# Optimization experiments

Hardware: AMD Instinct MI355X
Metric: run time of the kernel (lower is better)

## Reference

```python
import jax, jax.numpy as jnp
import numpy as np

S = 1024   # speakers_per_batch
U = 64     # utterances_per_speaker
D = 256    # embedding_size
EPS = 1e-5


def setup_inputs() -> dict:
    key = jax.random.key(0)
    k1, = jax.random.split(key, 1)
    return {
        "output_of_model": jax.random.normal(k1, (S * U, D), dtype=jnp.float32),
        "similarity_weight": jnp.array([10.0], dtype=jnp.float32),
        "similarity_bias": jnp.array([-5.0], dtype=jnp.float32),
        "speakers_per_batch": S,
        "utterances_per_speaker": U,
    }


def reference(output_of_model, similarity_weight, similarity_bias,
              speakers_per_batch, utterances_per_speaker):
    s, u = speakers_per_batch, utterances_per_speaker
    embeds = output_of_model.reshape(s, u, -1)                      # [S,U,D]

    # inclusive centroids (mean over utterances, L2-normalized with +eps)
    c_incl = jnp.mean(embeds, axis=1)                               # [S,D]
    c_incl = c_incl / (jnp.linalg.norm(c_incl, axis=-1, keepdims=True) + EPS)

    # exclusive centroids (leave-one-out mean, L2-normalized with +eps)
    c_excl = (jnp.sum(embeds, axis=1, keepdims=True) - embeds) / (u - 1)  # [S,U,D]
    c_excl = c_excl / (jnp.linalg.norm(c_excl, axis=-1, keepdims=True) + EPS)

    # normalized embeddings (original normalizes embeds inside the loop)
    e_n = embeds / (jnp.linalg.norm(embeds, axis=-1, keepdims=True) + EPS)

    # off-diagonal: cosine(embed[i,u], incl centroid[j]); diagonal: excl centroid
    sim_incl = jnp.einsum('sud,jd->suj', e_n, c_incl)               # [S,U,S]
    sim_excl = jnp.sum(e_n * c_excl, axis=-1)                       # [S,U]
    diag = jnp.eye(s, dtype=bool)[:, None, :]                       # [S,1,S]
    sim = jnp.where(diag, sim_excl[:, :, None], sim_incl)           # [S,U,S]

    sim = sim * similarity_weight + similarity_bias                 # scaled logits

    logits = sim.reshape(s * u, s)
    targets = jnp.repeat(jnp.arange(s), u)                          # ground truth
    logp = jax.nn.log_softmax(logits, axis=-1)
    loss = -jnp.mean(jnp.take_along_axis(logp, targets[:, None], axis=-1))
    return loss
```

## Files before the change

### kernel.cpp

```cpp
#include <hip/hip_runtime.h>

#define SPK 1024
#define UTT 64
#define DIM 256
#define EPSV 1e-5f
#define NROW (SPK * UTT)
#define NSL 8
#define LOG2E 1.44269504f

typedef __attribute__((ext_vector_type(4))) float f32x4;
typedef __attribute__((ext_vector_type(2))) long long2v;

#define EXP2(x) __builtin_amdgcn_exp2f(x)

__device__ __forceinline__ int pk_fp8(float a, float b, float c, float d) {
    int v = __builtin_amdgcn_cvt_pk_fp8_f32(a, b, 0, false);
    return  __builtin_amdgcn_cvt_pk_fp8_f32(c, d, v, true);
}

__device__ __forceinline__ int fragIdx(int g) {
    return ((g >> 4) * 4 + ((g & 7) >> 1)) * 4 + ((g >> 3) & 1) * 2 + (g & 1);
}

__global__ __launch_bounds__(256)
void k_prep(const float* __restrict__ x,
            unsigned char* __restrict__ cincl8,
            unsigned char* __restrict__ en8,
            float* __restrict__ texcl,
            const float* __restrict__ wp, const float* __restrict__ bp) {
    __shared__ float4 sc4[256];
    __shared__ float4 cs4[64];
    __shared__ float sccs;
    int s = blockIdx.x, tid = threadIdx.x;
    int dq = tid & 63, ug = tid >> 6;
    const float4* x4 = (const float4*)(x + (size_t)s * UTT * DIM);

    float4 p = {0.f, 0.f, 0.f, 0.f};
#pragma unroll
    for (int i = 0; i < 16; ++i) {
        float4 v = x4[(ug * 16 + i) * 64 + dq];
        p.x += v.x; p.y += v.y; p.z += v.z; p.w += v.w;
    }
    sc4[tid] = p;
    __syncthreads();
    if (tid < 64) {
        float4 a = sc4[dq], b2 = sc4[64 + dq], c = sc4[128 + dq], d = sc4[192 + dq];
        float4 cs = {a.x + b2.x + c.x + d.x, a.y + b2.y + c.y + d.y,
                     a.z + b2.z + c.z + d.z, a.w + b2.w + c.w + d.w};
        cs4[dq] = cs;
        float s2 = cs.x * cs.x + cs.y * cs.y + cs.z * cs.z + cs.w * cs.w;
#pragma unroll
        for (int o = 1; o < 64; o <<= 1) s2 += __shfl_xor(s2, o);
        if (tid == 0) sccs = s2;
        float inv = 16.f / (sqrtf(s2) + UTT * EPSV);
        ((int*)cincl8)[s * 64 + fragIdx(dq)] =
            pk_fp8(cs.x * inv, cs.y * inv, cs.z * inv, cs.w * inv);
    }
    __syncthreads();
    float scc = sccs;
    float w = wp[0], b = bp[0];

    int row = tid >> 2, sub = tid & 3;
    const float4* xr = x4 + row * 64;
    float4 xv[16];
    float sx = 0.f, sc = 0.f;
#pragma unroll
    for (int i = 0; i < 16; ++i) {
        float4 v = xr[i * 4 + sub];
        float4 cv = cs4[i * 4 + sub];
        xv[i] = v;
        sx += v.x * v.x + v.y * v.y + v.z * v.z + v.w * v.w;
        sc += v.x * cv.x + v.y * cv.y + v.z * cv.z + v.w * cv.w;
    }
    sx += __shfl_xor(sx, 1); sx += __shfl_xor(sx, 2);
    sc += __shfl_xor(sc, 1); sc += __shfl_xor(sc, 2);
    float nx = sqrtf(sx);
    float inv = 16.f / (nx + EPSV);
    int* er = (int*)(en8 + (size_t)(s * UTT + row) * DIM);
#pragma unroll
    for (int i = 0; i < 16; ++i)
        er[fragIdx(i * 4 + sub)] = pk_fp8(xv[i].x * inv, xv[i].y * inv,
                                          xv[i].z * inv, xv[i].w * inv);
    if (sub == 0) {
        float num = sc - sx;
        float e2 = fmaxf(scc - 2.f * sc + sx, 0.f);
        float sim = num / ((nx + EPSV) * (sqrtf(e2) + (UTT - 1) * EPSV));
        texcl[s * UTT + row] = fmaf(sim, w, b);
    }
}

__global__ __launch_bounds__(256, 3)
void k_main(const unsigned char* __restrict__ en8,
            const unsigned char* __restrict__ cincl8,
            float* __restrict__ partial,
            const float* __restrict__ wp, const float* __restrict__ bp) {
    __shared__ unsigned char Bs[32 * 1024];
    int tid = threadIdx.x, wave = tid >> 6, lane = tid & 63;
    int quad = lane >> 4, lx = lane & 15;
    int bid = blockIdx.x;
    int xcd = bid & 7, j = bid >> 3;
    int cs = j & 7;
    int sg = xcd + 8 * (j >> 3);
    int sw = sg * 4 + wave;
    float w = wp[0], b = bp[0];
    float M  = fabsf(w) * 1.0625f + b;
    float wl = w * (LOG2E / 256.f);
    float bl = (b - M) * LOG2E;

#pragma unroll
    for (int nti = 0; nti < 2; ++nti) {
        int nt = wave * 2 + nti;
#pragma unroll
        for (int r = 0; r < 4; ++r) {
            const unsigned char* g = cincl8 +
                (size_t)(cs * 128 + nt * 16 + lx) * DIM + (r * 4 + quad) * 16;
            __builtin_amdgcn_global_load_lds(
                (const __attribute__((address_space(1))) void*)g,
                (__attribute__((address_space(3))) void*)(Bs + (nt * 4 + r) * 1024),
                16, 0, 0);
        }
    }

    const unsigned char* abase = en8 + (size_t)sw * UTT * DIM;
    long2v af2[4][4];
#pragma unroll
    for (int mt = 0; mt < 4; ++mt)
#pragma unroll
        for (int r = 0; r < 4; ++r)
            af2[mt][r] = *(const long2v*)(abase + (mt * 16 + lx) * DIM + (r * 4 + quad) * 16);

    float l[16];
#pragma unroll
    for (int i = 0; i < 16; ++i) l[i] = 0.f;

    __syncthreads();

    int dnt = (sw >> 4) - cs * 8;
    int dlx = sw & 15;

    for (int nt = 0; nt < 8; ++nt) {
        long2v bf2[4];
#pragma unroll
        for (int r = 0; r < 4; ++r)
            bf2[r] = *(const long2v*)(Bs + (nt * 4 + r) * 1024 + lane * 16);
        f32x4 aA[4] = {{0.f,0.f,0.f,0.f},{0.f,0.f,0.f,0.f},
                       {0.f,0.f,0.f,0.f},{0.f,0.f,0.f,0.f}};
        f32x4 aB[4] = {{0.f,0.f,0.f,0.f},{0.f,0.f,0.f,0.f},
                       {0.f,0.f,0.f,0.f},{0.f,0.f,0.f,0.f}};
#pragma unroll
        for (int r = 0; r < 2; ++r) {
#pragma unroll
            for (int mt = 0; mt < 4; ++mt) {
                aA[mt] = __builtin_amdgcn_mfma_f32_16x16x32_fp8_fp8(af2[mt][r].x,   bf2[r].x,   aA[mt], 0, 0, 0);
                aB[mt] = __builtin_amdgcn_mfma_f32_16x16x32_fp8_fp8(af2[mt][r+2].x, bf2[r+2].x, aB[mt], 0, 0, 0);
            }
#pragma unroll
            for (int mt = 0; mt < 4; ++mt) {
                aA[mt] = __builtin_amdgcn_mfma_f32_16x16x32_fp8_fp8(af2[mt][r].y,   bf2[r].y,   aA[mt], 0, 0, 0);
                aB[mt] = __builtin_amdgcn_mfma_f32_16x16x32_fp8_fp8(af2[mt][r+2].y, bf2[r+2].y, aB[mt], 0, 0, 0);
            }
        }
#pragma unroll
        for (int mt = 0; mt < 4; ++mt)
#pragma unroll
            for (int r = 0; r < 4; ++r)
                l[mt * 4 + r] += EXP2(fmaf(aA[mt][r] + aB[mt][r], wl, bl));
        if (nt == dnt) {
#pragma unroll
            for (int mt = 0; mt < 4; ++mt)
#pragma unroll
                for (int r = 0; r < 4; ++r) {
                    float e = EXP2(fmaf(aA[mt][r] + aB[mt][r], wl, bl));
                    if (lx == dlx) l[mt * 4 + r] -= e;
                }
        }
    }

#pragma unroll
    for (int o = 1; o < 16; o <<= 1)
#pragma unroll
        for (int i = 0; i < 16; ++i) l[i] += __shfl_xor(l[i], o);
    if (lx == 0)
#pragma unroll
        for (int mt = 0; mt < 4; ++mt)
#pragma unroll
            for (int r = 0; r < 4; ++r)
                partial[(size_t)cs * NROW + (size_t)sw * UTT + mt * 16 + quad * 4 + r]
                    = l[mt * 4 + r];
}

__global__ __launch_bounds__(256)
void k_final(const float* __restrict__ partial, const float* __restrict__ texcl,
             const float* __restrict__ wp, const float* __restrict__ bp,
             float* __restrict__ out) {
    int row = blockIdx.x * 256 + threadIdx.x;
    float w = wp[0], b = bp[0];
    float M = fabsf(w) * 1.0625f + b;
    float t = 0.f;
#pragma unroll
    for (int sl = 0; sl < NSL; ++sl) t += partial[(size_t)sl * NROW + row];
    float tex = texcl[row];
    float c = (M + __logf(t + EXP2((tex - M) * LOG2E))) - tex;
#pragma unroll
    for (int o = 1; o < 64; o <<= 1) c += __shfl_xor(c, o);
    __shared__ float red[4];
    if ((threadIdx.x & 63) == 0) red[threadIdx.x >> 6] = c;
    __syncthreads();
    if (threadIdx.x == 0)
        atomicAdd(out, (red[0] + red[1] + red[2] + red[3]) * (1.f / NROW));
}

extern "C" void kernel_launch(void* const* d_in, const int* in_sizes, int n_in,
                              void* d_out, int out_size, void* d_ws, size_t ws_size,
                              hipStream_t stream) {
    const float* x  = (const float*)d_in[0];
    const float* wp = (const float*)d_in[1];
    const float* bp = (const float*)d_in[2];
    char* ws = (char*)d_ws;
    unsigned char* cincl8 = (unsigned char*)ws;
    float* texcl          = (float*)(ws + (1u << 19));
    float* partial        = (float*)(ws + (1u << 20));
    unsigned char* en8    = (unsigned char*)(ws + (4u << 20));
    float* out = (float*)d_out;

    hipMemsetAsync(d_out, 0, sizeof(float), stream);
    k_prep <<<SPK, 256, 0, stream>>>(x, cincl8, en8, texcl, wp, bp);
    k_main <<<(SPK / 4) * NSL, 256, 0, stream>>>(en8, cincl8, partial, wp, bp);
    k_final<<<NROW / 256, 256, 0, stream>>>(partial, texcl, wp, bp, out);
}
```

Baseline: 142.7 us.

## Fuse embedding normalization, GEMM and logsumexp into one kernel per speaker

Restructures the pipeline from prep/main/final into a centroid kernel plus a fused kernel. The fused kernel loads raw fp32 rows, computes norms and the exclusive similarity, and quantizes to fp8 in registers. It then streams all 1024 centroids through double-buffered LDS and finishes the log-softmax and loss reduction in place. This removes the fp8 embedding buffer round trip, the partial-sum array and the final kernel launch. In exchange, each block now handles only 64 rows with a single accumulator per wave, which gives less MFMA reuse and adds a sync per tile, and the input x is read from memory twice.

```diff
diff --git a/kernel.cpp b/kernel.cpp
--- a/kernel.cpp
+++ b/kernel.cpp
@@ -5,7 +5,6 @@
 #define DIM 256
 #define EPSV 1e-5f
 #define NROW (SPK * UTT)
-#define NSL 8
 #define LOG2E 1.44269504f
 
 typedef __attribute__((ext_vector_type(4))) float f32x4;
@@ -23,18 +22,12 @@
 }
 
 __global__ __launch_bounds__(256)
-void k_prep(const float* __restrict__ x,
-            unsigned char* __restrict__ cincl8,
-            unsigned char* __restrict__ en8,
-            float* __restrict__ texcl,
-            const float* __restrict__ wp, const float* __restrict__ bp) {
+void k_cent(const float* __restrict__ x, unsigned char* __restrict__ cincl8,
+            float* __restrict__ csum, float* __restrict__ nrm) {
     __shared__ float4 sc4[256];
-    __shared__ float4 cs4[64];
-    __shared__ float sccs;
     int s = blockIdx.x, tid = threadIdx.x;
     int dq = tid & 63, ug = tid >> 6;
     const float4* x4 = (const float4*)(x + (size_t)s * UTT * DIM);
-
     float4 p = {0.f, 0.f, 0.f, 0.f};
 #pragma unroll
     for (int i = 0; i < 16; ++i) {
@@ -47,166 +40,130 @@
         float4 a = sc4[dq], b2 = sc4[64 + dq], c = sc4[128 + dq], d = sc4[192 + dq];
         float4 cs = {a.x + b2.x + c.x + d.x, a.y + b2.y + c.y + d.y,
                      a.z + b2.z + c.z + d.z, a.w + b2.w + c.w + d.w};
-        cs4[dq] = cs;
+        ((float4*)csum)[s * 64 + dq] = cs;
         float s2 = cs.x * cs.x + cs.y * cs.y + cs.z * cs.z + cs.w * cs.w;
 #pragma unroll
         for (int o = 1; o < 64; o <<= 1) s2 += __shfl_xor(s2, o);
-        if (tid == 0) sccs = s2;
         float inv = 16.f / (sqrtf(s2) + UTT * EPSV);
         ((int*)cincl8)[s * 64 + fragIdx(dq)] =
             pk_fp8(cs.x * inv, cs.y * inv, cs.z * inv, cs.w * inv);
-    }
-    __syncthreads();
-    float scc = sccs;
-    float w = wp[0], b = bp[0];
-
-    int row = tid >> 2, sub = tid & 3;
-    const float4* xr = x4 + row * 64;
-    float4 xv[16];
-    float sx = 0.f, sc = 0.f;
-#pragma unroll
-    for (int i = 0; i < 16; ++i) {
-        float4 v = xr[i * 4 + sub];
-        float4 cv = cs4[i * 4 + sub];
-        xv[i] = v;
-        sx += v.x * v.x + v.y * v.y + v.z * v.z + v.w * v.w;
-        sc += v.x * cv.x + v.y * cv.y + v.z * cv.z + v.w * cv.w;
-    }
-    sx += __shfl_xor(sx, 1); sx += __shfl_xor(sx, 2);
-    sc += __shfl_xor(sc, 1); sc += __shfl_xor(sc, 2);
-    float nx = sqrtf(sx);
-    float inv = 16.f / (nx + EPSV);
-    int* er = (int*)(en8 + (size_t)(s * UTT + row) * DIM);
-#pragma unroll
-    for (int i = 0; i < 16; ++i)
-        er[fragIdx(i * 4 + sub)] = pk_fp8(xv[i].x * inv, xv[i].y * inv,
-                                          xv[i].z * inv, xv[i].w * inv);
-    if (sub == 0) {
-        float num = sc - sx;
-        float e2 = fmaxf(scc - 2.f * sc + sx, 0.f);
-        float sim = num / ((nx + EPSV) * (sqrtf(e2) + (UTT - 1) * EPSV));
-        texcl[s * UTT + row] = fmaf(sim, w, b);
+        if (tid == 0) nrm[s] = s2;
     }
 }
 
-__global__ __launch_bounds__(256, 3)
-void k_main(const unsigned char* __restrict__ en8,
-            const unsigned char* __restrict__ cincl8,
-            float* __restrict__ partial,
-            const float* __restrict__ wp, const float* __restrict__ bp) {
-    __shared__ unsigned char Bs[32 * 1024];
+__global__ __launch_bounds__(256, 2)
+void k_fused(const float* __restrict__ x, const unsigned char* __restrict__ cincl8,
+             const float* __restrict__ csum, const float* __restrict__ nrm,
+             const float* __restrict__ wp, const float* __restrict__ bp,
+             float* __restrict__ out) {
+    __shared__ unsigned char Bs[2][16 * 1024];
+    __shared__ float texs[64];
+    __shared__ float red[4];
     int tid = threadIdx.x, wave = tid >> 6, lane = tid & 63;
     int quad = lane >> 4, lx = lane & 15;
-    int bid = blockIdx.x;
-    int xcd = bid & 7, j = bid >> 3;
-    int cs = j & 7;
-    int sg = xcd + 8 * (j >> 3);
-    int sw = sg * 4 + wave;
+    int s = blockIdx.x;
     float w = wp[0], b = bp[0];
     float M  = fabsf(w) * 1.0625f + b;
     float wl = w * (LOG2E / 256.f);
     float bl = (b - M) * LOG2E;
 
+#define STAGE(buf, t)                                                           \
+    _Pragma("unroll")                                                           \
+    for (int r = 0; r < 4; ++r) {                                               \
+        const unsigned char* g = cincl8 +                                       \
+            (size_t)((t) * 64 + wave * 16 + lx) * DIM + (r * 4 + quad) * 16;    \
+        __builtin_amdgcn_global_load_lds(                                       \
+            (const __attribute__((address_space(1))) void*)g,                   \
+            (__attribute__((address_space(3))) void*)(Bs[buf] + (wave * 4 + r) * 1024), \
+            16, 0, 0);                                                          \
+    }
+    STAGE(0, 0);
+
+    int arow = wave * 16 + lx;
+    const float* xr = x + ((size_t)s * UTT + arow) * DIM + quad * 8;
+    const float* cb = csum + (size_t)s * DIM + quad * 8;
+    float4 xv[16];
+    float sx = 0.f, sc = 0.f;
 #pragma unroll
-    for (int nti = 0; nti < 2; ++nti) {
-        int nt = wave * 2 + nti;
+    for (int kt = 0; kt < 8; ++kt) {
+        float4 a0 = *(const float4*)(xr + kt * 32);
+        float4 a1 = *(const float4*)(xr + kt * 32 + 4);
+        float4 c0 = *(const float4*)(cb + kt * 32);
+        float4 c1 = *(const float4*)(cb + kt * 32 + 4);
+        xv[2 * kt] = a0; xv[2 * kt + 1] = a1;
+        sx += a0.x * a0.x + a0.y * a0.y + a0.z * a0.z + a0.w * a0.w
+            + a1.x * a1.x + a1.y * a1.y + a1.z * a1.z + a1.w * a1.w;
+        sc += a0.x * c0.x + a0.y * c0.y + a0.z * c0.z + a0.w * c0.w
+            + a1.x * c1.x + a1.y * c1.y + a1.z * c1.z + a1.w * c1.w;
+    }
+    sx += __shfl_xor(sx, 16); sx += __shfl_xor(sx, 32);
+    sc += __shfl_xor(sc, 16); sc += __shfl_xor(sc, 32);
+    float nx = sqrtf(sx);
+    float inv = 16.f / (nx + EPSV);
+    long af[8];
 #pragma unroll
-        for (int r = 0; r < 4; ++r) {
-            const unsigned char* g = cincl8 +
-                (size_t)(cs * 128 + nt * 16 + lx) * DIM + (r * 4 + quad) * 16;
-            __builtin_amdgcn_global_load_lds(
-                (const __attribute__((address_space(1))) void*)g,
-                (__attribute__((address_space(3))) void*)(Bs + (nt * 4 + r) * 1024),
-                16, 0, 0);
-        }
+    for (int kt = 0; kt < 8; ++kt) {
+        int lo = pk_fp8(xv[2 * kt].x * inv,     xv[2 * kt].y * inv,
+                        xv[2 * kt].z * inv,     xv[2 * kt].w * inv);
+        int hi = pk_fp8(xv[2 * kt + 1].x * inv, xv[2 * kt + 1].y * inv,
+                        xv[2 * kt + 1].z * inv, xv[2 * kt + 1].w * inv);
+        af[kt] = (long)(((unsigned long long)(unsigned)hi << 32) | (unsigned)lo);
+    }
+    if (quad == 0) {
+        float scc = nrm[s];
+        float num = sc - sx;
+        float e2 = fmaxf(scc - 2.f * sc + sx, 0.f);
+        float sim = num / ((nx + EPSV) * (sqrtf(e2) + (UTT - 1) * EPSV));
+        texs[arow] = fmaf(sim, w, b);
     }
 
-    const unsigned char* abase = en8 + (size_t)sw * UTT * DIM;
-    long2v af2[4][4];
-#pragma unroll
-    for (int mt = 0; mt < 4; ++mt)
-#pragma unroll
-        for (int r = 0; r < 4; ++r)
-            af2[mt][r] = *(const long2v*)(abase + (mt * 16 + lx) * DIM + (r * 4 + quad) * 16);
-
-    float l[16];
-#pragma unroll
-    for (int i = 0; i < 16; ++i) l[i] = 0.f;
-
+    float l[4] = {0.f, 0.f, 0.f, 0.f};
+    int s_hi = s >> 6, nt_d = (s >> 4) & 3, lx_d = s & 15;
     __syncthreads();
 
-    int dnt = (sw >> 4) - cs * 8;
-    int dlx = sw & 15;
-
-    for (int nt = 0; nt < 8; ++nt) {
-        long2v bf2[4];
+    for (int t = 0; t < 16; ++t) {
+        const unsigned char* bsc = Bs[t & 1];
+        if (t < 15) { STAGE((t & 1) ^ 1, t + 1); }
 #pragma unroll
-        for (int r = 0; r < 4; ++r)
-            bf2[r] = *(const long2v*)(Bs + (nt * 4 + r) * 1024 + lane * 16);
-        f32x4 aA[4] = {{0.f,0.f,0.f,0.f},{0.f,0.f,0.f,0.f},
-                       {0.f,0.f,0.f,0.f},{0.f,0.f,0.f,0.f}};
-        f32x4 aB[4] = {{0.f,0.f,0.f,0.f},{0.f,0.f,0.f,0.f},
-                       {0.f,0.f,0.f,0.f},{0.f,0.f,0.f,0.f}};
+        for (int nt = 0; nt < 4; ++nt) {
+            long2v bf2[4];
 #pragma unroll
-        for (int r = 0; r < 2; ++r) {
+            for (int r = 0; r < 4; ++r)
+                bf2[r] = *(const long2v*)(bsc + (nt * 4 + r) * 1024 + lane * 16);
+            f32x4 acc = {0.f, 0.f, 0.f, 0.f};
 #pragma unroll
-            for (int mt = 0; mt < 4; ++mt) {
-                aA[mt] = __builtin_amdgcn_mfma_f32_16x16x32_fp8_fp8(af2[mt][r].x,   bf2[r].x,   aA[mt], 0, 0, 0);
-                aB[mt] = __builtin_amdgcn_mfma_f32_16x16x32_fp8_fp8(af2[mt][r+2].x, bf2[r+2].x, aB[mt], 0, 0, 0);
+            for (int r = 0; r < 4; ++r) {
+                acc = __builtin_amdgcn_mfma_f32_16x16x32_fp8_fp8(af[2 * r],     bf2[r].x, acc, 0, 0, 0);
+                acc = __builtin_amdgcn_mfma_f32_16x16x32_fp8_fp8(af[2 * r + 1], bf2[r].y, acc, 0, 0, 0);
             }
+            bool dg = (t == s_hi) && (nt == nt_d);
 #pragma unroll
-            for (int mt = 0; mt < 4; ++mt) {
-                aA[mt] = __builtin_amdgcn_mfma_f32_16x16x32_fp8_fp8(af2[mt][r].y,   bf2[r].y,   aA[mt], 0, 0, 0);
-                aB[mt] = __builtin_amdgcn_mfma_f32_16x16x32_fp8_fp8(af2[mt][r+2].y, bf2[r+2].y, aB[mt], 0, 0, 0);
+            for (int i = 0; i < 4; ++i) {
+                float e = EXP2(fmaf(acc[i], wl, bl));
+                if (!(dg && lx == lx_d)) l[i] += e;
             }
         }
-#pragma unroll
-        for (int mt = 0; mt < 4; ++mt)
-#pragma unroll
-            for (int r = 0; r < 4; ++r)
-                l[mt * 4 + r] += EXP2(fmaf(aA[mt][r] + aB[mt][r], wl, bl));
-        if (nt == dnt) {
-#pragma unroll
-            for (int mt = 0; mt < 4; ++mt)
-#pragma unroll
-                for (int r = 0; r < 4; ++r) {
-                    float e = EXP2(fmaf(aA[mt][r] + aB[mt][r], wl, bl));
-                    if (lx == dlx) l[mt * 4 + r] -= e;
-                }
-        }
+        __syncthreads();
     }
 
 #pragma unroll
     for (int o = 1; o < 16; o <<= 1)
 #pragma unroll
-        for (int i = 0; i < 16; ++i) l[i] += __shfl_xor(l[i], o);
-    if (lx == 0)
+        for (int i = 0; i < 4; ++i) l[i] += __shfl_xor(l[i], o);
+
+    float cc = 0.f;
+    if (lx == 0) {
 #pragma unroll
-        for (int mt = 0; mt < 4; ++mt)
+        for (int i = 0; i < 4; ++i) {
+            float tex = texs[wave * 16 + quad * 4 + i];
+            cc += (M + __logf(l[i] + EXP2((tex - M) * LOG2E))) - tex;
+        }
+    }
 #pragma unroll
-            for (int r = 0; r < 4; ++r)
-                partial[(size_t)cs * NROW + (size_t)sw * UTT + mt * 16 + quad * 4 + r]
-                    = l[mt * 4 + r];
-}
-
-__global__ __launch_bounds__(256)
-void k_final(const float* __restrict__ partial, const float* __restrict__ texcl,
-             const float* __restrict__ wp, const float* __restrict__ bp,
-             float* __restrict__ out) {
-    int row = blockIdx.x * 256 + threadIdx.x;
-    float w = wp[0], b = bp[0];
-    float M = fabsf(w) * 1.0625f + b;
-    float t = 0.f;
-#pragma unroll
-    for (int sl = 0; sl < NSL; ++sl) t += partial[(size_t)sl * NROW + row];
-    float tex = texcl[row];
-    float c = (M + __logf(t + EXP2((tex - M) * LOG2E))) - tex;
-#pragma unroll
-    for (int o = 1; o < 64; o <<= 1) c += __shfl_xor(c, o);
-    __shared__ float red[4];
-    if ((threadIdx.x & 63) == 0) red[threadIdx.x >> 6] = c;
+    for (int o = 1; o < 64; o <<= 1) cc += __shfl_xor(cc, o);
+    if (lane == 0) red[wave] = cc;
     __syncthreads();
-    if (threadIdx.x == 0)
+    if (tid == 0)
         atomicAdd(out, (red[0] + red[1] + red[2] + red[3]) * (1.f / NROW));
 }
 
@@ -218,13 +175,11 @@
     const float* bp = (const float*)d_in[2];
     char* ws = (char*)d_ws;
     unsigned char* cincl8 = (unsigned char*)ws;
-    float* texcl          = (float*)(ws + (1u << 19));
-    float* partial        = (float*)(ws + (1u << 20));
-    unsigned char* en8    = (unsigned char*)(ws + (4u << 20));
+    float* csum           = (float*)(ws + (1u << 19));
+    float* nrm            = (float*)(ws + (2u << 20));
     float* out = (float*)d_out;
 
     hipMemsetAsync(d_out, 0, sizeof(float), stream);
-    k_prep <<<SPK, 256, 0, stream>>>(x, cincl8, en8, texcl, wp, bp);
-    k_main <<<(SPK / 4) * NSL, 256, 0, stream>>>(en8, cincl8, partial, wp, bp);
-    k_final<<<NROW / 256, 256, 0, stream>>>(partial, texcl, wp, bp, out);
+    k_cent <<<SPK, 256, 0, stream>>>(x, cincl8, csum, nrm);
+    k_fused<<<SPK, 256, 0, stream>>>(x, cincl8, csum, nrm, wp, bp, out);
 }
```

New measurement: 144.9 us. About the same (+1.6%).

## Restructure main GEMM tiling to stream centroids from global and reuse prep loads

Applied to the files above, without the earlier changes.

k_main now assigns one speaker's 64 rows to every wave of a block and splits the centroid columns across waves and two halves. Centroid fragments are loaded straight from global memory with a one-step register prefetch, so the LDS staging and block barrier are gone. k_prep keeps the first-pass loads in registers and computes row norms with wave-wide shuffles instead of reloading x, which removes the second global read. The trade-offs are that every wave re-reads the A tile and B is fetched from L2 without LDS sharing. The new prep uses many more shuffles, and launch bounds change to allow 4 blocks for prep and 2 for main.

```diff
diff --git a/kernel.cpp b/kernel.cpp
--- a/kernel.cpp
+++ b/kernel.cpp
@@ -22,23 +22,25 @@
     return ((g >> 4) * 4 + ((g & 7) >> 1)) * 4 + ((g >> 3) & 1) * 2 + (g & 1);
 }
 
-__global__ __launch_bounds__(256)
+__global__ __launch_bounds__(256, 4)
 void k_prep(const float* __restrict__ x,
             unsigned char* __restrict__ cincl8,
             unsigned char* __restrict__ en8,
             float* __restrict__ texcl,
             const float* __restrict__ wp, const float* __restrict__ bp) {
     __shared__ float4 sc4[256];
-    __shared__ float4 cs4[64];
+    __shared__ float4 csq[64];
     __shared__ float sccs;
     int s = blockIdx.x, tid = threadIdx.x;
     int dq = tid & 63, ug = tid >> 6;
     const float4* x4 = (const float4*)(x + (size_t)s * UTT * DIM);
 
+    float4 xv[16];
     float4 p = {0.f, 0.f, 0.f, 0.f};
 #pragma unroll
     for (int i = 0; i < 16; ++i) {
         float4 v = x4[(ug * 16 + i) * 64 + dq];
+        xv[i] = v;
         p.x += v.x; p.y += v.y; p.z += v.z; p.w += v.w;
     }
     sc4[tid] = p;
@@ -47,102 +49,92 @@
         float4 a = sc4[dq], b2 = sc4[64 + dq], c = sc4[128 + dq], d = sc4[192 + dq];
         float4 cs = {a.x + b2.x + c.x + d.x, a.y + b2.y + c.y + d.y,
                      a.z + b2.z + c.z + d.z, a.w + b2.w + c.w + d.w};
-        cs4[dq] = cs;
+        csq[dq] = cs;
         float s2 = cs.x * cs.x + cs.y * cs.y + cs.z * cs.z + cs.w * cs.w;
 #pragma unroll
         for (int o = 1; o < 64; o <<= 1) s2 += __shfl_xor(s2, o);
-        if (tid == 0) sccs = s2;
         float inv = 16.f / (sqrtf(s2) + UTT * EPSV);
         ((int*)cincl8)[s * 64 + fragIdx(dq)] =
             pk_fp8(cs.x * inv, cs.y * inv, cs.z * inv, cs.w * inv);
+        if (tid == 0) sccs = s2;
     }
     __syncthreads();
     float scc = sccs;
+    float4 cv = csq[dq];
     float w = wp[0], b = bp[0];
 
-    int row = tid >> 2, sub = tid & 3;
-    const float4* xr = x4 + row * 64;
-    float4 xv[16];
-    float sx = 0.f, sc = 0.f;
+    float sxl[16], scl[16];
 #pragma unroll
     for (int i = 0; i < 16; ++i) {
-        float4 v = xr[i * 4 + sub];
-        float4 cv = cs4[i * 4 + sub];
-        xv[i] = v;
-        sx += v.x * v.x + v.y * v.y + v.z * v.z + v.w * v.w;
-        sc += v.x * cv.x + v.y * cv.y + v.z * cv.z + v.w * cv.w;
-    }
-    sx += __shfl_xor(sx, 1); sx += __shfl_xor(sx, 2);
-    sc += __shfl_xor(sc, 1); sc += __shfl_xor(sc, 2);
-    float nx = sqrtf(sx);
-    float inv = 16.f / (nx + EPSV);
-    int* er = (int*)(en8 + (size_t)(s * UTT + row) * DIM);
-#pragma unroll
-    for (int i = 0; i < 16; ++i)
-        er[fragIdx(i * 4 + sub)] = pk_fp8(xv[i].x * inv, xv[i].y * inv,
-                                          xv[i].z * inv, xv[i].w * inv);
-    if (sub == 0) {
-        float num = sc - sx;
-        float e2 = fmaxf(scc - 2.f * sc + sx, 0.f);
-        float sim = num / ((nx + EPSV) * (sqrtf(e2) + (UTT - 1) * EPSV));
-        texcl[s * UTT + row] = fmaf(sim, w, b);
-    }
-}
-
-__global__ __launch_bounds__(256, 3)
+        float4 v = xv[i];
+        sxl[i] = v.x * v.x + v.y * v.y + v.z * v.z + v.w * v.w;
+        scl[i] = v.x * cv.x + v.y * cv.y + v.z * cv.z + v.w * cv.w;
+    }
+#pragma unroll
+    for (int o = 1; o < 64; o <<= 1)
+#pragma unroll
+        for (int i = 0; i < 16; ++i) {
+            sxl[i] += __shfl_xor(sxl[i], o);
+            scl[i] += __shfl_xor(scl[i], o);
+        }
+    int fi = fragIdx(dq);
+#pragma unroll
+    for (int i = 0; i < 16; ++i) {
+        float inv = 16.f / (sqrtf(sxl[i]) + EPSV);
+        ((int*)(en8 + (size_t)(s * UTT + ug * 16 + i) * DIM))[fi] =
+            pk_fp8(xv[i].x * inv, xv[i].y * inv, xv[i].z * inv, xv[i].w * inv);
+    }
+    if (dq == 0) {
+#pragma unroll
+        for (int i = 0; i < 16; ++i) {
+            float nx = sqrtf(sxl[i]);
+            float num = scl[i] - sxl[i];
+            float e2 = fmaxf(scc - 2.f * scl[i] + sxl[i], 0.f);
+            float sim = num / ((nx + EPSV) * (sqrtf(e2) + (UTT - 1) * EPSV));
+            texcl[s * UTT + ug * 16 + i] = fmaf(sim, w, b);
+        }
+    }
+}
+
+__global__ __launch_bounds__(256, 2)
 void k_main(const unsigned char* __restrict__ en8,
             const unsigned char* __restrict__ cincl8,
             float* __restrict__ partial,
             const float* __restrict__ wp, const float* __restrict__ bp) {
-    __shared__ unsigned char Bs[32 * 1024];
     int tid = threadIdx.x, wave = tid >> 6, lane = tid & 63;
     int quad = lane >> 4, lx = lane & 15;
     int bid = blockIdx.x;
-    int xcd = bid & 7, j = bid >> 3;
-    int cs = j & 7;
-    int sg = xcd + 8 * (j >> 3);
-    int sw = sg * 4 + wave;
+    int s = bid & (SPK - 1), h = bid >> 10;
     float w = wp[0], b = bp[0];
     float M  = fabsf(w) * 1.0625f + b;
     float wl = w * (LOG2E / 256.f);
     float bl = (b - M) * LOG2E;
 
-#pragma unroll
-    for (int nti = 0; nti < 2; ++nti) {
-        int nt = wave * 2 + nti;
-#pragma unroll
-        for (int r = 0; r < 4; ++r) {
-            const unsigned char* g = cincl8 +
-                (size_t)(cs * 128 + nt * 16 + lx) * DIM + (r * 4 + quad) * 16;
-            __builtin_amdgcn_global_load_lds(
-                (const __attribute__((address_space(1))) void*)g,
-                (__attribute__((address_space(3))) void*)(Bs + (nt * 4 + r) * 1024),
-                16, 0, 0);
-        }
-    }
-
-    const unsigned char* abase = en8 + (size_t)sw * UTT * DIM;
-    long2v af2[4][4];
+    const unsigned char* abase = en8 + (size_t)s * UTT * DIM;
+    long2v af[4][4];
 #pragma unroll
     for (int mt = 0; mt < 4; ++mt)
 #pragma unroll
         for (int r = 0; r < 4; ++r)
-            af2[mt][r] = *(const long2v*)(abase + (mt * 16 + lx) * DIM + (r * 4 + quad) * 16);
+            af[mt][r] = *(const long2v*)(abase + (mt * 16 + lx) * DIM + (r * 4 + quad) * 16);
 
     float l[16];
 #pragma unroll
     for (int i = 0; i < 16; ++i) l[i] = 0.f;
-
-    __syncthreads();
-
-    int dnt = (sw >> 4) - cs * 8;
-    int dlx = sw & 15;
-
-    for (int nt = 0; nt < 8; ++nt) {
-        long2v bf2[4];
+    int t_d = s >> 6, w_d = (s >> 4) & 3, lx_d = s & 15;
+    const unsigned char* bp_ = cincl8 + (size_t)(wave * 16 + lx) * DIM + quad * 16;
+
+    long2v bfc[4], bfn[4];
+    int t0 = h * 8;
+#pragma unroll
+    for (int r = 0; r < 4; ++r)
+        bfc[r] = *(const long2v*)(bp_ + (size_t)(t0 * 64) * DIM + r * 64);
+
+    for (int t = t0; t < t0 + 8; ++t) {
+        const unsigned char* bn = bp_ + (size_t)(((t + 1) & 15) * 64) * DIM;
 #pragma unroll
         for (int r = 0; r < 4; ++r)
-            bf2[r] = *(const long2v*)(Bs + (nt * 4 + r) * 1024 + lane * 16);
+            bfn[r] = *(const long2v*)(bn + r * 64);
         f32x4 aA[4] = {{0.f,0.f,0.f,0.f},{0.f,0.f,0.f,0.f},
                        {0.f,0.f,0.f,0.f},{0.f,0.f,0.f,0.f}};
         f32x4 aB[4] = {{0.f,0.f,0.f,0.f},{0.f,0.f,0.f,0.f},
@@ -151,29 +143,31 @@
         for (int r = 0; r < 2; ++r) {
 #pragma unroll
             for (int mt = 0; mt < 4; ++mt) {
-                aA[mt] = __builtin_amdgcn_mfma_f32_16x16x32_fp8_fp8(af2[mt][r].x,   bf2[r].x,   aA[mt], 0, 0, 0);
-                aB[mt] = __builtin_amdgcn_mfma_f32_16x16x32_fp8_fp8(af2[mt][r+2].x, bf2[r+2].x, aB[mt], 0, 0, 0);
+                aA[mt] = __builtin_amdgcn_mfma_f32_16x16x32_fp8_fp8(af[mt][r].x,   bfc[r].x,   aA[mt], 0, 0, 0);
+                aB[mt] = __builtin_amdgcn_mfma_f32_16x16x32_fp8_fp8(af[mt][r+2].x, bfc[r+2].x, aB[mt], 0, 0, 0);
             }
 #pragma unroll
             for (int mt = 0; mt < 4; ++mt) {
-                aA[mt] = __builtin_amdgcn_mfma_f32_16x16x32_fp8_fp8(af2[mt][r].y,   bf2[r].y,   aA[mt], 0, 0, 0);
-                aB[mt] = __builtin_amdgcn_mfma_f32_16x16x32_fp8_fp8(af2[mt][r+2].y, bf2[r+2].y, aB[mt], 0, 0, 0);
+                aA[mt] = __builtin_amdgcn_mfma_f32_16x16x32_fp8_fp8(af[mt][r].y,   bfc[r].y,   aA[mt], 0, 0, 0);
+                aB[mt] = __builtin_amdgcn_mfma_f32_16x16x32_fp8_fp8(af[mt][r+2].y, bfc[r+2].y, aB[mt], 0, 0, 0);
             }
         }
 #pragma unroll
         for (int mt = 0; mt < 4; ++mt)
 #pragma unroll
-            for (int r = 0; r < 4; ++r)
-                l[mt * 4 + r] += EXP2(fmaf(aA[mt][r] + aB[mt][r], wl, bl));
-        if (nt == dnt) {
+            for (int i = 0; i < 4; ++i)
+                l[mt * 4 + i] += EXP2(fmaf(aA[mt][i] + aB[mt][i], wl, bl));
+        if (t == t_d && wave == w_d) {
 #pragma unroll
             for (int mt = 0; mt < 4; ++mt)
 #pragma unroll
-                for (int r = 0; r < 4; ++r) {
-                    float e = EXP2(fmaf(aA[mt][r] + aB[mt][r], wl, bl));
-                    if (lx == dlx) l[mt * 4 + r] -= e;
+                for (int i = 0; i < 4; ++i) {
+                    float e = EXP2(fmaf(aA[mt][i] + aB[mt][i], wl, bl));
+                    if (lx == lx_d) l[mt * 4 + i] -= e;
                 }
         }
+#pragma unroll
+        for (int r = 0; r < 4; ++r) bfc[r] = bfn[r];
     }
 
 #pragma unroll
@@ -184,9 +178,9 @@
 #pragma unroll
         for (int mt = 0; mt < 4; ++mt)
 #pragma unroll
-            for (int r = 0; r < 4; ++r)
-                partial[(size_t)cs * NROW + (size_t)sw * UTT + mt * 16 + quad * 4 + r]
-                    = l[mt * 4 + r];
+            for (int i = 0; i < 4; ++i)
+                partial[(size_t)(h * 4 + wave) * NROW + (size_t)s * UTT
+                        + mt * 16 + quad * 4 + i] = l[mt * 4 + i];
 }
 
 __global__ __launch_bounds__(256)
@@ -225,6 +219,6 @@
 
     hipMemsetAsync(d_out, 0, sizeof(float), stream);
     k_prep <<<SPK, 256, 0, stream>>>(x, cincl8, en8, texcl, wp, bp);
-    k_main <<<(SPK / 4) * NSL, 256, 0, stream>>>(en8, cincl8, partial, wp, bp);
+    k_main <<<2 * SPK, 256, 0, stream>>>(en8, cincl8, partial, wp, bp);
     k_final<<<NROW / 256, 256, 0, stream>>>(partial, texcl, wp, bp, out);
 }
```

Result: slower. 173.3 us (+21.5%).

## Reuse first-pass loads in prep kernel and stage fp8 output through LDS

Applied to the files above, without the earlier changes.

The prep kernel now keeps the 16 float4 values each thread loads during the centroid-sum pass, instead of reading every row of x a second time. Per-row norms and centroid dot products are computed with a full 64-lane butterfly reduction across 16 rows at once. The packed fp8 values are transposed through a padded LDS buffer so that each row is written to global memory as contiguous 16-byte stores. This removes the second global read of the input and the scattered 4-byte stores. In exchange it adds about 17 KB of LDS, many more shuffles, and an extra barrier, and the kernel now requests two blocks per SM.

```diff
diff --git a/kernel.cpp b/kernel.cpp
--- a/kernel.cpp
+++ b/kernel.cpp
@@ -22,23 +22,26 @@
     return ((g >> 4) * 4 + ((g & 7) >> 1)) * 4 + ((g >> 3) & 1) * 2 + (g & 1);
 }
 
-__global__ __launch_bounds__(256)
+__global__ __launch_bounds__(256, 2)
 void k_prep(const float* __restrict__ x,
             unsigned char* __restrict__ cincl8,
             unsigned char* __restrict__ en8,
             float* __restrict__ texcl,
             const float* __restrict__ wp, const float* __restrict__ bp) {
     __shared__ float4 sc4[256];
-    __shared__ float4 cs4[64];
+    __shared__ float4 csq[64];
     __shared__ float sccs;
+    __shared__ int tr[64 * 68];
     int s = blockIdx.x, tid = threadIdx.x;
     int dq = tid & 63, ug = tid >> 6;
     const float4* x4 = (const float4*)(x + (size_t)s * UTT * DIM);
 
+    float4 xv[16];
     float4 p = {0.f, 0.f, 0.f, 0.f};
 #pragma unroll
     for (int i = 0; i < 16; ++i) {
         float4 v = x4[(ug * 16 + i) * 64 + dq];
+        xv[i] = v;
         p.x += v.x; p.y += v.y; p.z += v.z; p.w += v.w;
     }
     sc4[tid] = p;
@@ -47,46 +50,58 @@
         float4 a = sc4[dq], b2 = sc4[64 + dq], c = sc4[128 + dq], d = sc4[192 + dq];
         float4 cs = {a.x + b2.x + c.x + d.x, a.y + b2.y + c.y + d.y,
                      a.z + b2.z + c.z + d.z, a.w + b2.w + c.w + d.w};
-        cs4[dq] = cs;
+        csq[dq] = cs;
         float s2 = cs.x * cs.x + cs.y * cs.y + cs.z * cs.z + cs.w * cs.w;
 #pragma unroll
         for (int o = 1; o < 64; o <<= 1) s2 += __shfl_xor(s2, o);
-        if (tid == 0) sccs = s2;
         float inv = 16.f / (sqrtf(s2) + UTT * EPSV);
         ((int*)cincl8)[s * 64 + fragIdx(dq)] =
             pk_fp8(cs.x * inv, cs.y * inv, cs.z * inv, cs.w * inv);
+        if (tid == 0) sccs = s2;
     }
     __syncthreads();
     float scc = sccs;
+    float4 cv = csq[dq];
     float w = wp[0], b = bp[0];
 
-    int row = tid >> 2, sub = tid & 3;
-    const float4* xr = x4 + row * 64;
-    float4 xv[16];
-    float sx = 0.f, sc = 0.f;
+    float sxl[16], scl[16];
 #pragma unroll
     for (int i = 0; i < 16; ++i) {
-        float4 v = xr[i * 4 + sub];
-        float4 cv = cs4[i * 4 + sub];
-        xv[i] = v;
-        sx += v.x * v.x + v.y * v.y + v.z * v.z + v.w * v.w;
-        sc += v.x * cv.x + v.y * cv.y + v.z * cv.z + v.w * cv.w;
-    }
-    sx += __shfl_xor(sx, 1); sx += __shfl_xor(sx, 2);
-    sc += __shfl_xor(sc, 1); sc += __shfl_xor(sc, 2);
-    float nx = sqrtf(sx);
-    float inv = 16.f / (nx + EPSV);
-    int* er = (int*)(en8 + (size_t)(s * UTT + row) * DIM);
-#pragma unroll
-    for (int i = 0; i < 16; ++i)
-        er[fragIdx(i * 4 + sub)] = pk_fp8(xv[i].x * inv, xv[i].y * inv,
-                                          xv[i].z * inv, xv[i].w * inv);
-    if (sub == 0) {
-        float num = sc - sx;
-        float e2 = fmaxf(scc - 2.f * sc + sx, 0.f);
-        float sim = num / ((nx + EPSV) * (sqrtf(e2) + (UTT - 1) * EPSV));
-        texcl[s * UTT + row] = fmaf(sim, w, b);
-    }
+        float4 v = xv[i];
+        sxl[i] = v.x * v.x + v.y * v.y + v.z * v.z + v.w * v.w;
+        scl[i] = v.x * cv.x + v.y * cv.y + v.z * cv.z + v.w * cv.w;
+    }
+#pragma unroll
+    for (int o = 1; o < 64; o <<= 1)
+#pragma unroll
+        for (int i = 0; i < 16; ++i) {
+            sxl[i] += __shfl_xor(sxl[i], o);
+            scl[i] += __shfl_xor(scl[i], o);
+        }
+    int fi = fragIdx(dq);
+#pragma unroll
+    for (int i = 0; i < 16; ++i) {
+        float inv = 16.f / (sqrtf(sxl[i]) + EPSV);
+        tr[(ug * 16 + i) * 68 + fi] =
+            pk_fp8(xv[i].x * inv, xv[i].y * inv, xv[i].z * inv, xv[i].w * inv);
+    }
+    if (dq == 0) {
+#pragma unroll
+        for (int i = 0; i < 16; ++i) {
+            float nx = sqrtf(sxl[i]);
+            float num = scl[i] - sxl[i];
+            float e2 = fmaxf(scc - 2.f * scl[i] + sxl[i], 0.f);
+            float sim = num / ((nx + EPSV) * (sqrtf(e2) + (UTT - 1) * EPSV));
+            texcl[s * UTT + ug * 16 + i] = fmaf(sim, w, b);
+        }
+    }
+    __syncthreads();
+    int row = tid >> 2, ch = tid & 3;
+    unsigned char* gout = en8 + (size_t)(s * UTT + row) * DIM + ch * 64;
+    const int* lsrc = &tr[row * 68 + ch * 16];
+#pragma unroll
+    for (int k = 0; k < 4; ++k)
+        *(int4*)(gout + k * 16) = *(const int4*)(lsrc + k * 4);
 }
 
 __global__ __launch_bounds__(256, 3)
```

New measurement: 144.5 us. About the same (+1.2%).
